# Performance work log

Measured on AMD Instinct MI355X. Metric: run time of the kernel, lower is better.

The kernel has to match this reference:

```python
import jax, jax.numpy as jnp
import numpy as np


def setup_inputs() -> dict:
    key = jax.random.key(0)
    kq, kk, kv = jax.random.split(key, 3)
    B, H, S, D = 4, 16, 2048, 64
    q = jax.random.normal(kq, (B, H, S, D), dtype=jnp.float32)
    k = jax.random.normal(kk, (B, H, S, D), dtype=jnp.float32)
    v = jax.random.normal(kv, (B, H, S, D), dtype=jnp.float32)
    return {"q": q, "k": k, "v": v}


def reference(q, k, v):
    # scale = sqrt(d_k); source's self.scale is undefined, standard SDPA scaling assumed
    scale = jnp.asarray(np.sqrt(q.shape[-1]), dtype=q.dtype)
    # [B,H,S,S] scores; sigmoid instead of softmax (no normalization across keys)
    scores = jnp.einsum("bhqd,bhkd->bhqk", q, k) / scale
    attn = jax.nn.sigmoid(scores)
    return jnp.einsum("bhqk,bhkd->bhqd", attn, v)
```

## Files before the change

kernel.cpp:

```cpp
#include <hip/hip_runtime.h>


typedef __bf16 bf16_t;
typedef __attribute__((ext_vector_type(8))) __bf16 bf16x8;
typedef __attribute__((ext_vector_type(4))) __bf16 bf16x4;
typedef __attribute__((ext_vector_type(4))) float  f32x4;

#if defined(__HIP_DEVICE_COMPILE__) && __has_builtin(__builtin_amdgcn_exp2f)
#define FAST_EXP2(x) __builtin_amdgcn_exp2f(x)
#else
#define FAST_EXP2(x) exp2f(x)
#endif
#if defined(__HIP_DEVICE_COMPILE__) && __has_builtin(__builtin_amdgcn_rcpf)
#define FAST_RCP(x) __builtin_amdgcn_rcpf(x)
#else
#define FAST_RCP(x) (1.0f/(x))
#endif

static constexpr int SEQ = 2048;
static constexpr int DH  = 64;
static constexpr int KB  = 32;
static constexpr int NIT = SEQ / KB;
static constexpr int QPW = 64;
static constexpr int QPB = 256;
static constexpr int CHUNK = 4096;

__global__ __launch_bounds__(256)
void sigattn_prepass(const float* __restrict__ Kg, const float* __restrict__ Vg,
                     bf16_t* __restrict__ ws)
{
    const int bh = blockIdx.x, it = blockIdx.y;
    const int t  = threadIdx.x;
    const int kb = it * KB;
    const size_t hbase = (size_t)bh * SEQ * DH;
    bf16_t* wbase = ws + ((size_t)bh * NIT + it) * CHUNK;

    {
        const int f = t >> 6, lane = t & 63;
        const int ks = f >> 1, dh = f & 1, c16 = lane & 15, g4 = lane >> 4;
        const float* p = Kg + hbase + (size_t)(kb + ks * 16 + c16) * DH + dh * 32 + g4 * 8;
        f32x4 a = *(const f32x4*)p;
        f32x4 b = *(const f32x4*)(p + 4);
        bf16x8 o;
        o[0] = (bf16_t)a.x; o[1] = (bf16_t)a.y; o[2] = (bf16_t)a.z; o[3] = (bf16_t)a.w;
        o[4] = (bf16_t)b.x; o[5] = (bf16_t)b.y; o[6] = (bf16_t)b.z; o[7] = (bf16_t)b.w;
        *(bf16x8*)&wbase[(size_t)t * 8] = o;
    }
    {
        const int c = t & 63, rblk = t >> 6;
        const int dt = c >> 4, c16 = c & 15;
        const float* p = Vg + hbase + (size_t)(kb + rblk * 8) * DH + c;
        float v[8];
        #pragma unroll
        for (int i = 0; i < 8; ++i) v[i] = p[(size_t)i * DH];
        const int j0  = (rblk >> 1) * 4;
        const int g4a = (rblk & 1) * 2;
        bf16x4 ca, cb;
        #pragma unroll
        for (int i = 0; i < 4; ++i) { ca[i] = (bf16_t)v[i]; cb[i] = (bf16_t)v[4 + i]; }
        bf16_t* vr = wbase + 2048;
        *(bf16x4*)&vr[(size_t)(dt * 64 + g4a * 16 + c16) * 8 + j0]       = ca;
        *(bf16x4*)&vr[(size_t)(dt * 64 + (g4a + 1) * 16 + c16) * 8 + j0] = cb;
    }
}

__global__ __launch_bounds__(256, 2)
void sigattn_main(const float* __restrict__ Qg, const bf16_t* __restrict__ ws,
                  float* __restrict__ Og)
{
    __shared__ __align__(16) bf16_t buf[2][CHUNK];

    const int t    = threadIdx.x;
    const int wave = t >> 6;
    const int lane = t & 63;
    const int c16  = lane & 15;
    const int g4   = lane >> 4;

    const int bh    = blockIdx.x;
    const int qtile = blockIdx.y;

    const float* Qp = Qg + (size_t)bh * SEQ * DH;
    float*       Op = Og + (size_t)bh * SEQ * DH;
    const bf16_t* wsh = ws + (size_t)bh * NIT * CHUNK;

    const int qwave = qtile * QPB + wave * QPW;

    const float qscale = -0.125f * 1.44269504088896340736f;
    bf16x8 qf[4][2];
    #pragma unroll
    for (int qs = 0; qs < 4; ++qs) {
        #pragma unroll
        for (int dh = 0; dh < 2; ++dh) {
            const float* p = Qp + (size_t)(qwave + qs * 16 + c16) * DH + dh * 32 + g4 * 8;
            f32x4 a = *(const f32x4*)p;
            f32x4 b = *(const f32x4*)(p + 4);
            bf16x8 f;
            f[0] = (bf16_t)(a.x * qscale); f[1] = (bf16_t)(a.y * qscale);
            f[2] = (bf16_t)(a.z * qscale); f[3] = (bf16_t)(a.w * qscale);
            f[4] = (bf16_t)(b.x * qscale); f[5] = (bf16_t)(b.y * qscale);
            f[6] = (bf16_t)(b.z * qscale); f[7] = (bf16_t)(b.w * qscale);
            qf[qs][dh] = f;
        }
    }

    bf16x8 rK, rV;
    auto gload = [&](int it) {
        const bf16_t* g = wsh + (size_t)it * CHUNK + t * 8;
        rK = *(const bf16x8*)g;
        rV = *(const bf16x8*)(g + 2048);
    };
    auto lstore = [&](int nb) {
        *(bf16x8*)&buf[nb][t * 8]        = rK;
        *(bf16x8*)&buf[nb][2048 + t * 8] = rV;
    };

    gload(0);
    lstore(0);

    f32x4 acc[4][4] = {};

    for (int it = 0; it < NIT; ++it) {
        const int cur = it & 1;
        __syncthreads();
        if (it + 1 < NIT) gload(it + 1);

        bf16x8 kf[4], vf[4];
        #pragma unroll
        for (int f = 0; f < 4; ++f) kf[f] = *(const bf16x8*)&buf[cur][(f * 64 + lane) * 8];
        #pragma unroll
        for (int f = 0; f < 4; ++f) vf[f] = *(const bf16x8*)&buf[cur][2048 + (f * 64 + lane) * 8];

        #pragma unroll
        for (int qs = 0; qs < 4; ++qs) {
            f32x4 s0 = {0.f, 0.f, 0.f, 0.f}, s1 = {0.f, 0.f, 0.f, 0.f};
            s0 = __builtin_amdgcn_mfma_f32_16x16x32_bf16(kf[0], qf[qs][0], s0, 0, 0, 0);
            s0 = __builtin_amdgcn_mfma_f32_16x16x32_bf16(kf[1], qf[qs][1], s0, 0, 0, 0);
            s1 = __builtin_amdgcn_mfma_f32_16x16x32_bf16(kf[2], qf[qs][0], s1, 0, 0, 0);
            s1 = __builtin_amdgcn_mfma_f32_16x16x32_bf16(kf[3], qf[qs][1], s1, 0, 0, 0);
            bf16x8 p8;
            #pragma unroll
            for (int r = 0; r < 4; ++r) p8[r]     = (bf16_t)FAST_RCP(1.0f + FAST_EXP2(s0[r]));
            #pragma unroll
            for (int r = 0; r < 4; ++r) p8[4 + r] = (bf16_t)FAST_RCP(1.0f + FAST_EXP2(s1[r]));
            #pragma unroll
            for (int dt = 0; dt < 4; ++dt)
                acc[qs][dt] = __builtin_amdgcn_mfma_f32_16x16x32_bf16(p8, vf[dt], acc[qs][dt], 0, 0, 0);
        }

        if (it + 1 < NIT) lstore(cur ^ 1);
    }

    #pragma unroll
    for (int qs = 0; qs < 4; ++qs) {
        const int q0 = qwave + qs * 16 + g4 * 4;
        #pragma unroll
        for (int r = 0; r < 4; ++r) {
            float* po = Op + (size_t)(q0 + r) * DH + c16;
            po[0]  = acc[qs][0][r];
            po[16] = acc[qs][1][r];
            po[32] = acc[qs][2][r];
            po[48] = acc[qs][3][r];
        }
    }
}

__global__ __launch_bounds__(256, 4)
void sigattn_fallback(const float* __restrict__ Qg, const float* __restrict__ Kg,
                      const float* __restrict__ Vg, float* __restrict__ Og)
{
    __shared__ bf16_t Kbuf[2][4 * 64 * 8];
    __shared__ bf16_t Vbuf[2][4 * 64 * 8];
    const int t = threadIdx.x, wave = t >> 6, lane = t & 63;
    const int c16 = lane & 15, g4 = lane >> 4;
    const int bh = blockIdx.x, qtile = blockIdx.y;
    const size_t hbase = (size_t)bh * SEQ * DH;
    const float* Qp = Qg + hbase; const float* Kp = Kg + hbase;
    const float* Vp = Vg + hbase; float* Op = Og + hbase;
    const int qwave = qtile * 128 + wave * 32;
    const float qscale = -0.125f * 1.44269504088896340736f;
    bf16x8 qf[2][2];
    #pragma unroll
    for (int qs = 0; qs < 2; ++qs)
        #pragma unroll
        for (int dh = 0; dh < 2; ++dh) {
            const float* p = Qp + (size_t)(qwave + qs * 16 + c16) * DH + dh * 32 + g4 * 8;
            f32x4 a = *(const f32x4*)p; f32x4 b = *(const f32x4*)(p + 4);
            bf16x8 f;
            f[0]=(bf16_t)(a.x*qscale); f[1]=(bf16_t)(a.y*qscale); f[2]=(bf16_t)(a.z*qscale); f[3]=(bf16_t)(a.w*qscale);
            f[4]=(bf16_t)(b.x*qscale); f[5]=(bf16_t)(b.y*qscale); f[6]=(bf16_t)(b.z*qscale); f[7]=(bf16_t)(b.w*qscale);
            qf[qs][dh] = f;
        }
    f32x4 kst0, kst1; float vst[8];
    auto issue_loads = [&](int kb0) {
        const float* pk = Kp + (size_t)(kb0 + (wave >> 1) * 16 + c16) * DH + (wave & 1) * 32 + g4 * 8;
        kst0 = *(const f32x4*)pk; kst1 = *(const f32x4*)(pk + 4);
        const float* pv = Vp + (size_t)(kb0 + g4 * 4) * DH + wave * 16 + c16;
        #pragma unroll
        for (int h = 0; h < 2; ++h)
            #pragma unroll
            for (int j = 0; j < 4; ++j) vst[h * 4 + j] = pv[(size_t)(h * 16 + j) * DH];
    };
    auto store_lds = [&](int buf) {
        bf16x8 k8;
        k8[0]=(bf16_t)kst0.x; k8[1]=(bf16_t)kst0.y; k8[2]=(bf16_t)kst0.z; k8[3]=(bf16_t)kst0.w;
        k8[4]=(bf16_t)kst1.x; k8[5]=(bf16_t)kst1.y; k8[6]=(bf16_t)kst1.z; k8[7]=(bf16_t)kst1.w;
        *(bf16x8*)&Kbuf[buf][t * 8] = k8;
        bf16x8 v8;
        #pragma unroll
        for (int j = 0; j < 8; ++j) v8[j] = (bf16_t)vst[j];
        *(bf16x8*)&Vbuf[buf][t * 8] = v8;
    };
    issue_loads(0); store_lds(0);
    f32x4 acc[2][4] = {};
    for (int it = 0; it < NIT; ++it) {
        const int buf = it & 1;
        __syncthreads();
        if (it + 1 < NIT) issue_loads((it + 1) * KB);
        bf16x8 kf[4], vf[4];
        #pragma unroll
        for (int f = 0; f < 4; ++f) kf[f] = *(const bf16x8*)&Kbuf[buf][(f * 64 + lane) * 8];
        #pragma unroll
        for (int f = 0; f < 4; ++f) vf[f] = *(const bf16x8*)&Vbuf[buf][(f * 64 + lane) * 8];
        #pragma unroll
        for (int qs = 0; qs < 2; ++qs) {
            f32x4 s0 = {0.f,0.f,0.f,0.f}, s1 = {0.f,0.f,0.f,0.f};
            s0 = __builtin_amdgcn_mfma_f32_16x16x32_bf16(kf[0], qf[qs][0], s0, 0, 0, 0);
            s0 = __builtin_amdgcn_mfma_f32_16x16x32_bf16(kf[1], qf[qs][1], s0, 0, 0, 0);
            s1 = __builtin_amdgcn_mfma_f32_16x16x32_bf16(kf[2], qf[qs][0], s1, 0, 0, 0);
            s1 = __builtin_amdgcn_mfma_f32_16x16x32_bf16(kf[3], qf[qs][1], s1, 0, 0, 0);
            bf16x8 p8;
            #pragma unroll
            for (int r = 0; r < 4; ++r) p8[r]     = (bf16_t)FAST_RCP(1.0f + FAST_EXP2(s0[r]));
            #pragma unroll
            for (int r = 0; r < 4; ++r) p8[4 + r] = (bf16_t)FAST_RCP(1.0f + FAST_EXP2(s1[r]));
            #pragma unroll
            for (int dt = 0; dt < 4; ++dt)
                acc[qs][dt] = __builtin_amdgcn_mfma_f32_16x16x32_bf16(p8, vf[dt], acc[qs][dt], 0, 0, 0);
        }
        if (it + 1 < NIT) store_lds(buf ^ 1);
    }
    #pragma unroll
    for (int qs = 0; qs < 2; ++qs) {
        const int q0 = qwave + qs * 16 + g4 * 4;
        #pragma unroll
        for (int r = 0; r < 4; ++r) {
            float* po = Op + (size_t)(q0 + r) * DH + c16;
            po[0]  = acc[qs][0][r];
            po[16] = acc[qs][1][r];
            po[32] = acc[qs][2][r];
            po[48] = acc[qs][3][r];
        }
    }
}

extern "C" void kernel_launch(void* const* d_in, const int* in_sizes, int n_in,
                              void* d_out, int out_size, void* d_ws, size_t ws_size,
                              hipStream_t stream)
{
    const float* q = (const float*)d_in[0];
    const float* k = (const float*)d_in[1];
    const float* v = (const float*)d_in[2];
    float* o = (float*)d_out;
    const size_t need = 64ull * NIT * CHUNK * sizeof(bf16_t);
    if (ws_size >= need) {
        sigattn_prepass<<<dim3(64, NIT), dim3(256), 0, stream>>>(k, v, (bf16_t*)d_ws);
        sigattn_main<<<dim3(64, SEQ / QPB), dim3(256), 0, stream>>>(q, (const bf16_t*)d_ws, o);
    } else {
        sigattn_fallback<<<dim3(64, SEQ / 128), dim3(256), 0, stream>>>(q, k, v, o);
    }
}
```

Measured before the change: 207.2 us.

## Load K/V fragments directly from global into registers, drop LDS staging

```diff
diff --git a/kernel.cpp b/kernel.cpp
--- a/kernel.cpp
+++ b/kernel.cpp
@@ -5,6 +5,7 @@
 typedef __attribute__((ext_vector_type(8))) __bf16 bf16x8;
 typedef __attribute__((ext_vector_type(4))) __bf16 bf16x4;
 typedef __attribute__((ext_vector_type(4))) float  f32x4;
+typedef __attribute__((ext_vector_type(4))) unsigned u32x4;
 
 #if defined(__HIP_DEVICE_COMPILE__) && __has_builtin(__builtin_amdgcn_exp2f)
 #define FAST_EXP2(x) __builtin_amdgcn_exp2f(x)
@@ -17,6 +18,16 @@
 #define FAST_RCP(x) (1.0f/(x))
 #endif
 
+static __device__ __forceinline__ unsigned pack_bf16(float a, float b) {
+#if defined(__HIP_DEVICE_COMPILE__) && __has_builtin(__builtin_amdgcn_perm)
+    return __builtin_amdgcn_perm(__builtin_bit_cast(unsigned, b),
+                                 __builtin_bit_cast(unsigned, a), 0x07060302u);
+#else
+    return (__builtin_bit_cast(unsigned, a) >> 16) |
+           (__builtin_bit_cast(unsigned, b) & 0xffff0000u);
+#endif
+}
+
 static constexpr int SEQ = 2048;
 static constexpr int DH  = 64;
 static constexpr int KB  = 32;
@@ -68,8 +79,6 @@
 void sigattn_main(const float* __restrict__ Qg, const bf16_t* __restrict__ ws,
                   float* __restrict__ Og)
 {
-    __shared__ __align__(16) bf16_t buf[2][CHUNK];
-
     const int t    = threadIdx.x;
     const int wave = t >> 6;
     const int lane = t & 63;
@@ -103,33 +112,17 @@
         }
     }
 
-    bf16x8 rK, rV;
-    auto gload = [&](int it) {
-        const bf16_t* g = wsh + (size_t)it * CHUNK + t * 8;
-        rK = *(const bf16x8*)g;
-        rV = *(const bf16x8*)(g + 2048);
-    };
-    auto lstore = [&](int nb) {
-        *(bf16x8*)&buf[nb][t * 8]        = rK;
-        *(bf16x8*)&buf[nb][2048 + t * 8] = rV;
-    };
-
-    gload(0);
-    lstore(0);
+    auto load_frags = [&](bf16x8* kf, bf16x8* vf, int it) {
+        const bf16_t* g = wsh + (size_t)it * CHUNK + (size_t)lane * 8;
+        #pragma unroll
+        for (int f = 0; f < 4; ++f) kf[f] = *(const bf16x8*)(g + f * 512);
+        #pragma unroll
+        for (int f = 0; f < 4; ++f) vf[f] = *(const bf16x8*)(g + 2048 + f * 512);
+    };
 
     f32x4 acc[4][4] = {};
 
-    for (int it = 0; it < NIT; ++it) {
-        const int cur = it & 1;
-        __syncthreads();
-        if (it + 1 < NIT) gload(it + 1);
-
-        bf16x8 kf[4], vf[4];
-        #pragma unroll
-        for (int f = 0; f < 4; ++f) kf[f] = *(const bf16x8*)&buf[cur][(f * 64 + lane) * 8];
-        #pragma unroll
-        for (int f = 0; f < 4; ++f) vf[f] = *(const bf16x8*)&buf[cur][2048 + (f * 64 + lane) * 8];
-
+    auto compute = [&](const bf16x8* kf, const bf16x8* vf) {
         #pragma unroll
         for (int qs = 0; qs < 4; ++qs) {
             f32x4 s0 = {0.f, 0.f, 0.f, 0.f}, s1 = {0.f, 0.f, 0.f, 0.f};
@@ -137,17 +130,33 @@
             s0 = __builtin_amdgcn_mfma_f32_16x16x32_bf16(kf[1], qf[qs][1], s0, 0, 0, 0);
             s1 = __builtin_amdgcn_mfma_f32_16x16x32_bf16(kf[2], qf[qs][0], s1, 0, 0, 0);
             s1 = __builtin_amdgcn_mfma_f32_16x16x32_bf16(kf[3], qf[qs][1], s1, 0, 0, 0);
-            bf16x8 p8;
-            #pragma unroll
-            for (int r = 0; r < 4; ++r) p8[r]     = (bf16_t)FAST_RCP(1.0f + FAST_EXP2(s0[r]));
-            #pragma unroll
-            for (int r = 0; r < 4; ++r) p8[4 + r] = (bf16_t)FAST_RCP(1.0f + FAST_EXP2(s1[r]));
+            float p0 = FAST_RCP(1.0f + FAST_EXP2(s0[0]));
+            float p1 = FAST_RCP(1.0f + FAST_EXP2(s0[1]));
+            float p2 = FAST_RCP(1.0f + FAST_EXP2(s0[2]));
+            float p3 = FAST_RCP(1.0f + FAST_EXP2(s0[3]));
+            float p4 = FAST_RCP(1.0f + FAST_EXP2(s1[0]));
+            float p5 = FAST_RCP(1.0f + FAST_EXP2(s1[1]));
+            float p6 = FAST_RCP(1.0f + FAST_EXP2(s1[2]));
+            float p7 = FAST_RCP(1.0f + FAST_EXP2(s1[3]));
+            u32x4 pu;
+            pu.x = pack_bf16(p0, p1);
+            pu.y = pack_bf16(p2, p3);
+            pu.z = pack_bf16(p4, p5);
+            pu.w = pack_bf16(p6, p7);
+            bf16x8 p8 = __builtin_bit_cast(bf16x8, pu);
             #pragma unroll
             for (int dt = 0; dt < 4; ++dt)
                 acc[qs][dt] = __builtin_amdgcn_mfma_f32_16x16x32_bf16(p8, vf[dt], acc[qs][dt], 0, 0, 0);
         }
-
-        if (it + 1 < NIT) lstore(cur ^ 1);
+    };
+
+    bf16x8 kA[4], vA[4], kB[4], vB[4];
+    load_frags(kA, vA, 0);
+    for (int it = 0; it < NIT; it += 2) {
+        load_frags(kB, vB, it + 1);
+        compute(kA, vA);
+        if (it + 2 < NIT) load_frags(kA, vA, it + 2);
+        compute(kB, vB);
     }
 
     #pragma unroll
```

New measurement: 209.7 us. About the same (+1.3%).
